# Kernel optimization log

Hardware: AMD Instinct MI355X
Metric: run time of the kernel (lower is better)

## Reference

```python
import jax, jax.numpy as jnp
import numpy as np

EPS = 1e-5

def _segment_mean(src_feat, edge_index, num_targets):
    # src_feat: [Ns, D]; edge_index: [2, E] = [source_idx, target_idx]
    msgs = src_feat[edge_index[0]]                                   # [E, D] gather
    agg = jax.ops.segment_sum(msgs, edge_index[1], num_segments=num_targets)
    deg = jax.ops.segment_sum(jnp.ones((edge_index.shape[1],), src_feat.dtype),
                              edge_index[1], num_segments=num_targets)
    return agg / jnp.clip(deg, 1.0)[:, None]

def _layernorm(x, gamma, beta):
    mu = jnp.mean(x, axis=-1, keepdims=True)
    var = jnp.mean(jnp.square(x - mu), axis=-1, keepdims=True)
    return (x - mu) * jax.lax.rsqrt(var + EPS) * gamma + beta

def setup_inputs() -> dict:
    key = jax.random.key(0)
    ks = jax.random.split(key, 8)
    NU, NI, E, D = 50000, 50000, 300000, 256
    s = 1.0 / np.sqrt(D)
    return {
        "user_features": jax.random.normal(ks[0], (NU, D), jnp.float32),
        "item_features": jax.random.normal(ks[1], (NI, D), jnp.float32),
        "user_item_edge_index": jax.random.randint(ks[2], (2, E), 0, NI),
        "item_user_edge_index": jax.random.randint(ks[3], (2, E), 0, NU),
        "Wu": jax.random.uniform(ks[4], (D, D), jnp.float32, -s, s),
        "bu": jax.random.uniform(ks[5], (D,), jnp.float32, -s, s),
        "Wi": jax.random.uniform(ks[6], (D, D), jnp.float32, -s, s),
        "bi": jax.random.uniform(ks[7], (D,), jnp.float32, -s, s),
        "gamma": jnp.ones((D,), jnp.float32),
        "beta": jnp.zeros((D,), jnp.float32),
    }

def reference(user_features, item_features, user_item_edge_index, item_user_edge_index,
              Wu, bu, Wi, bi, gamma, beta):
    num_items = item_features.shape[0]
    num_users = user_features.shape[0]
    # messages into items come from users; into users come from items
    item_messages = _segment_mean(user_features, user_item_edge_index, num_items)
    user_messages = _segment_mean(item_features, item_user_edge_index, num_users)
    u_new = (user_features + user_messages) @ Wu + bu
    i_new = (item_features + item_messages) @ Wi + bi
    u_new = _layernorm(jax.nn.relu(u_new), gamma, beta)
    i_new = _layernorm(jax.nn.relu(i_new), gamma, beta)
    return (u_new, i_new)
```

## Files before the change

### kernel.cpp

```cpp
#include <hip/hip_runtime.h>
#include <hip/hip_bf16.h>

#define D 256
#define BM 64
#define BK2 32
#define LDK2 40
#define LDK 72

typedef __attribute__((ext_vector_type(8))) __bf16 bf16x8;
typedef __attribute__((ext_vector_type(4))) float f32x4;

__device__ __forceinline__ float bf2f(unsigned short u) {
    union { unsigned int i; float f; } c; c.i = ((unsigned int)u) << 16; return c.f;
}
__device__ __forceinline__ float bf2f_lo(unsigned int u) {
    union { unsigned int i; float f; } c; c.i = u << 16; return c.f;
}
__device__ __forceinline__ float bf2f_hi(unsigned int u) {
    union { unsigned int i; float f; } c; c.i = u & 0xffff0000u; return c.f;
}
__device__ __forceinline__ unsigned short f2bf(float f) {
    __hip_bfloat16 h = __float2bfloat16(f);
    return *reinterpret_cast<unsigned short*>(&h);
}
__device__ __forceinline__ unsigned int pack2(float lo, float hi) {
    return (unsigned int)f2bf(lo) | ((unsigned int)f2bf(hi) << 16);
}


__global__ void k_cvt_all(const float* __restrict__ uf, const float* __restrict__ itf,
                          const float* __restrict__ Wu, const float* __restrict__ Wi,
                          unsigned short* __restrict__ feat_bf,
                          unsigned short* __restrict__ Wt_u, unsigned short* __restrict__ Wt_i,
                          int* __restrict__ deg, int Ntot,
                          size_t nfU, size_t nfTot, int nbF) {
    int b = blockIdx.x;
    if (b < nbF) {
        size_t base = ((size_t)b * 256 + threadIdx.x) * 8;
        if (base < nfTot) {
            const float* s = (base < nfU) ? (uf + base) : (itf + (base - nfU));
            float4 f0 = *(const float4*)s;
            float4 f1 = *(const float4*)(s + 4);
            ushort4 o0, o1;
            o0.x = f2bf(f0.x); o0.y = f2bf(f0.y); o0.z = f2bf(f0.z); o0.w = f2bf(f0.w);
            o1.x = f2bf(f1.x); o1.y = f2bf(f1.y); o1.z = f2bf(f1.z); o1.w = f2bf(f1.w);
            ((ushort4*)(feat_bf + base))[0] = o0;
            ((ushort4*)(feat_bf + base))[1] = o1;
        }
    } else if (b < nbF + 512) {
        int b2 = b - nbF;
        const float* W = (b2 < 256) ? Wu : Wi;
        unsigned short* Wt = (b2 < 256) ? Wt_u : Wt_i;
        int k = b2 & 255;
        int c = threadIdx.x;
        Wt[(size_t)c * 256 + k] = f2bf(W[(size_t)k * 256 + c]);
    } else {
        int zb = b - nbF - 512;
        size_t base = ((size_t)zb * 256 + threadIdx.x) * 4;
        if (base + 4 <= (size_t)Ntot) {
            *(int4*)(deg + base) = make_int4(0, 0, 0, 0);
        } else if (base < (size_t)Ntot) {
            for (size_t j = base; j < (size_t)Ntot; ++j) deg[j] = 0;
        }
    }
}

__global__ void k_hist2(const int* __restrict__ iu_e, int Eiu,
                        const int* __restrict__ ui_e, int Eui,
                        int* __restrict__ deg, int NU) {
    int e = blockIdx.x * blockDim.x + threadIdx.x;
    if (e < Eiu) {
        atomicAdd(&deg[iu_e[Eiu + e]], 1);
    } else if (e < Eiu + Eui) {
        int e2 = e - Eiu;
        atomicAdd(&deg[NU + ui_e[Eui + e2]], 1);
    }
}

__global__ void k_scan_block(const int* __restrict__ deg, int N,
                             int* __restrict__ rs, int* __restrict__ bsums) {
    __shared__ int s[1024];
    int base = blockIdx.x * 1024;
    int t = threadIdx.x;
    int v = (base + t < N) ? deg[base + t] : 0;
    s[t] = v;
    __syncthreads();
    for (int off = 1; off < 1024; off <<= 1) {
        int add = (t >= off) ? s[t - off] : 0;
        __syncthreads();
        s[t] += add;
        __syncthreads();
    }
    if (base + t < N) rs[base + t + 1] = s[t];
    if (t == 1023) bsums[blockIdx.x] = s[1023];
}

__global__ void k_scan_sums(int* __restrict__ bsums, int nb) {
    __shared__ int s[1024];
    int t = threadIdx.x;
    int v = (t < nb) ? bsums[t] : 0;
    s[t] = v;
    __syncthreads();
    for (int off = 1; off < 1024; off <<= 1) {
        int add = (t >= off) ? s[t - off] : 0;
        __syncthreads();
        s[t] += add;
        __syncthreads();
    }
    if (t < nb) bsums[t] = s[t] - v;
}

__global__ void k_finalize(int N, int* __restrict__ rs, int* __restrict__ cur,
                           const int* __restrict__ bsums) {
    int i = blockIdx.x * blockDim.x + threadIdx.x;
    if (i < N) {
        int v = rs[i + 1] + bsums[i >> 10];
        rs[i + 1] = v;
        cur[i + 1] = v;
    }
    if (i == 0) { rs[0] = 0; cur[0] = 0; }
}

__global__ void k_fill2(const int* __restrict__ iu_e, int Eiu,
                        const int* __restrict__ ui_e, int Eui,
                        int* __restrict__ cur, int NU,
                        int* __restrict__ csr) {
    int e = blockIdx.x * blockDim.x + threadIdx.x;
    if (e < Eiu) {
        int d = iu_e[Eiu + e];
        int p = atomicAdd(&cur[d], 1);
        csr[p] = iu_e[e];
    } else if (e < Eiu + Eui) {
        int e2 = e - Eiu;
        int d = ui_e[Eui + e2];
        int p = atomicAdd(&cur[NU + d], 1);
        csr[p] = ui_e[e2];
    }
}

__global__ void k_msg2(const unsigned short* __restrict__ uf_bf,
                       const unsigned short* __restrict__ if_bf,
                       const int* __restrict__ rs, const int* __restrict__ csr,
                       unsigned short* __restrict__ x_u, unsigned short* __restrict__ x_i,
                       int NU, int NI) {
    int pair = (blockIdx.x * blockDim.x + threadIdx.x) >> 6;
    int lane = threadIdx.x & 63;
    int half = lane >> 5;
    int hl   = lane & 31;
    int Ntot = NU + NI;
    int wv = pair * 2 + half;
    if (wv >= Ntot) return;

    const unsigned short* src; const unsigned short* tgt; unsigned short* xo; int w;
    if (wv < NU) { src = if_bf; tgt = uf_bf; xo = x_u; w = wv; }
    else         { src = uf_bf; tgt = if_bf; xo = x_i; w = wv - NU; }

    int s0 = rs[wv], s1 = rs[wv + 1];
    float a0[8] = {}, a1[8] = {}, a2[8] = {}, a3[8] = {};

    int i = s0;
    for (; i + 4 <= s1; i += 4) {
        int e0 = csr[i], e1 = csr[i + 1], e2 = csr[i + 2], e3 = csr[i + 3];
        uint4 r0 = ((const uint4*)(src + (size_t)e0 * D))[hl];
        uint4 r1 = ((const uint4*)(src + (size_t)e1 * D))[hl];
        uint4 r2 = ((const uint4*)(src + (size_t)e2 * D))[hl];
        uint4 r3 = ((const uint4*)(src + (size_t)e3 * D))[hl];
        a0[0] += bf2f_lo(r0.x); a0[1] += bf2f_hi(r0.x); a0[2] += bf2f_lo(r0.y); a0[3] += bf2f_hi(r0.y);
        a0[4] += bf2f_lo(r0.z); a0[5] += bf2f_hi(r0.z); a0[6] += bf2f_lo(r0.w); a0[7] += bf2f_hi(r0.w);
        a1[0] += bf2f_lo(r1.x); a1[1] += bf2f_hi(r1.x); a1[2] += bf2f_lo(r1.y); a1[3] += bf2f_hi(r1.y);
        a1[4] += bf2f_lo(r1.z); a1[5] += bf2f_hi(r1.z); a1[6] += bf2f_lo(r1.w); a1[7] += bf2f_hi(r1.w);
        a2[0] += bf2f_lo(r2.x); a2[1] += bf2f_hi(r2.x); a2[2] += bf2f_lo(r2.y); a2[3] += bf2f_hi(r2.y);
        a2[4] += bf2f_lo(r2.z); a2[5] += bf2f_hi(r2.z); a2[6] += bf2f_lo(r2.w); a2[7] += bf2f_hi(r2.w);
        a3[0] += bf2f_lo(r3.x); a3[1] += bf2f_hi(r3.x); a3[2] += bf2f_lo(r3.y); a3[3] += bf2f_hi(r3.y);
        a3[4] += bf2f_lo(r3.z); a3[5] += bf2f_hi(r3.z); a3[6] += bf2f_lo(r3.w); a3[7] += bf2f_hi(r3.w);
    }
    for (; i < s1; ++i) {
        int e0 = csr[i];
        uint4 r0 = ((const uint4*)(src + (size_t)e0 * D))[hl];
        a0[0] += bf2f_lo(r0.x); a0[1] += bf2f_hi(r0.x); a0[2] += bf2f_lo(r0.y); a0[3] += bf2f_hi(r0.y);
        a0[4] += bf2f_lo(r0.z); a0[5] += bf2f_hi(r0.z); a0[6] += bf2f_lo(r0.w); a0[7] += bf2f_hi(r0.w);
    }

    int cnt = s1 - s0;
    float inv = 1.0f / (float)(cnt > 0 ? cnt : 1);
    uint4 tv = ((const uint4*)(tgt + (size_t)w * D))[hl];
    float x0 = bf2f_lo(tv.x) + (a0[0] + a1[0] + a2[0] + a3[0]) * inv;
    float x1 = bf2f_hi(tv.x) + (a0[1] + a1[1] + a2[1] + a3[1]) * inv;
    float x2 = bf2f_lo(tv.y) + (a0[2] + a1[2] + a2[2] + a3[2]) * inv;
    float x3 = bf2f_hi(tv.y) + (a0[3] + a1[3] + a2[3] + a3[3]) * inv;
    float x4 = bf2f_lo(tv.z) + (a0[4] + a1[4] + a2[4] + a3[4]) * inv;
    float x5 = bf2f_hi(tv.z) + (a0[5] + a1[5] + a2[5] + a3[5]) * inv;
    float x6 = bf2f_lo(tv.w) + (a0[6] + a1[6] + a2[6] + a3[6]) * inv;
    float x7 = bf2f_hi(tv.w) + (a0[7] + a1[7] + a2[7] + a3[7]) * inv;
    uint4 o;
    o.x = pack2(x0, x1); o.y = pack2(x2, x3); o.z = pack2(x4, x5); o.w = pack2(x6, x7);
    ((uint4*)(xo + (size_t)w * D))[hl] = o;
}

__launch_bounds__(256)
__global__ void k_gemm2(const unsigned short* __restrict__ x_u,
                        const unsigned short* __restrict__ x_i,
                        const unsigned short* __restrict__ Wt_u,
                        const unsigned short* __restrict__ Wt_i,
                        const float* __restrict__ bu, const float* __restrict__ bi,
                        const float* __restrict__ gamma, const float* __restrict__ beta,
                        int NU, int NI, int nbU, float* __restrict__ out) {
    __shared__ __hip_bfloat16 As[BM][LDK2];
    __shared__ __hip_bfloat16 Bs[D][LDK2];
    __shared__ float red_s[BM][4];
    __shared__ float red_q[BM][4];

    int b = blockIdx.x;
    bool isU = b < nbU;
    const unsigned short* X  = isU ? x_u : x_i;
    const unsigned short* Wt = isU ? Wt_u : Wt_i;
    const float* bias        = isU ? bu : bi;
    float* Y                 = isU ? out : out + (size_t)NU * D;
    int N                    = isU ? NU : NI;
    int row0 = (isU ? b : b - nbU) * BM;

    int t = threadIdx.x;
    int lane = t & 63;
    int w = t >> 6;
    int l15 = lane & 15;
    int l4 = lane >> 4;

    int ar = row0 + (t >> 2);
    int ak = (t & 3) * 8;
    const uint4* Ag = (const uint4*)&X[(size_t)ar * D + ak];
    const uint4* Bg = (const uint4*)&Wt[(size_t)t * D];

    uint4 uz = {0, 0, 0, 0};
    bool aok = (ar < N);
    uint4 aR = aok ? Ag[0] : uz;
    uint4 bR0 = Bg[0], bR1 = Bg[1], bR2 = Bg[2], bR3 = Bg[3];

    f32x4 acc[4][4];
    f32x4 zero = {0.f, 0.f, 0.f, 0.f};
    #pragma unroll
    for (int fr = 0; fr < 4; fr++)
        #pragma unroll
        for (int fc = 0; fc < 4; fc++)
            acc[fr][fc] = zero;

    for (int k0 = 0; k0 < D; k0 += BK2) {
        *(uint4*)&As[t >> 2][ak] = aR;
        *(uint4*)&Bs[t][0]  = bR0;
        *(uint4*)&Bs[t][8]  = bR1;
        *(uint4*)&Bs[t][16] = bR2;
        *(uint4*)&Bs[t][24] = bR3;
        __syncthreads();
        if (k0 + BK2 < D) {
            int kn = (k0 + BK2) >> 3;
            aR  = aok ? Ag[kn] : uz;
            bR0 = Bg[kn]; bR1 = Bg[kn + 1]; bR2 = Bg[kn + 2]; bR3 = Bg[kn + 3];
        }
        bf16x8 af[4], bg4[4];
        #pragma unroll
        for (int fr = 0; fr < 4; fr++)
            af[fr] = *(const bf16x8*)&As[fr * 16 + l15][l4 * 8];
        #pragma unroll
        for (int fc = 0; fc < 4; fc++)
            bg4[fc] = *(const bf16x8*)&Bs[w * 64 + fc * 16 + l15][l4 * 8];
        #pragma unroll
        for (int fr = 0; fr < 4; fr++)
            #pragma unroll
            for (int fc = 0; fc < 4; fc++)
                acc[fr][fc] = __builtin_amdgcn_mfma_f32_16x16x32_bf16(
                    af[fr], bg4[fc], acc[fr][fc], 0, 0, 0);
        __syncthreads();
    }

    float bias_c[4], gam_c[4], bet_c[4];
    #pragma unroll
    for (int fc = 0; fc < 4; fc++) {
        int col = w * 64 + fc * 16 + l15;
        bias_c[fc] = bias[col];
        gam_c[fc]  = gamma[col];
        bet_c[fc]  = beta[col];
    }

    #pragma unroll
    for (int fr = 0; fr < 4; fr++) {
        #pragma unroll
        for (int r = 0; r < 4; r++) {
            int row = fr * 16 + l4 * 4 + r;
            float s = 0.f, q = 0.f;
            #pragma unroll
            for (int fc = 0; fc < 4; fc++) {
                float v = acc[fr][fc][r] + bias_c[fc];
                v = fmaxf(v, 0.f);
                acc[fr][fc][r] = v;
                s += v;
                q += v * v;
            }
            #pragma unroll
            for (int m = 1; m < 16; m <<= 1) {
                s += __shfl_xor(s, m);
                q += __shfl_xor(q, m);
            }
            if (l15 == 0) { red_s[row][w] = s; red_q[row][w] = q; }
        }
    }
    __syncthreads();

    #pragma unroll
    for (int fr = 0; fr < 4; fr++) {
        #pragma unroll
        for (int r = 0; r < 4; r++) {
            int row = fr * 16 + l4 * 4 + r;
            int grow = row0 + row;
            if (grow >= N) continue;
            float s = red_s[row][0] + red_s[row][1] + red_s[row][2] + red_s[row][3];
            float q = red_q[row][0] + red_q[row][1] + red_q[row][2] + red_q[row][3];
            float mu  = s * (1.0f / 256.0f);
            float var = q * (1.0f / 256.0f) - mu * mu;
            float rstd = rsqrtf(var + 1e-5f);
            #pragma unroll
            for (int fc = 0; fc < 4; fc++) {
                int col = w * 64 + fc * 16 + l15;
                Y[(size_t)grow * D + col] = (acc[fr][fc][r] - mu) * rstd * gam_c[fc] + bet_c[fc];
            }
        }
    }
}


__global__ void k_hist(const int* __restrict__ dst, int E, int* __restrict__ deg) {
    int e = blockIdx.x * blockDim.x + threadIdx.x;
    if (e < E) atomicAdd(&deg[dst[e]], 1);
}

__global__ void k_finalize_rs(int N, int* __restrict__ rs, const int* __restrict__ bsums) {
    int i = blockIdx.x * blockDim.x + threadIdx.x;
    if (i < N) rs[i + 1] += bsums[i >> 10];
    if (i == 0) rs[0] = 0;
}

__global__ void k_fill(const int* __restrict__ src, const int* __restrict__ dst, int E,
                       const int* __restrict__ rs, int* __restrict__ cursor,
                       int* __restrict__ csr) {
    int e = blockIdx.x * blockDim.x + threadIdx.x;
    if (e < E) {
        int d = dst[e];
        int p = atomicAdd(&cursor[d], 1);
        csr[rs[d] + p] = src[e];
    }
}

__global__ void k_msg_x(const float* __restrict__ srcf, const float* __restrict__ tgtf,
                        const int* __restrict__ rs, const int* __restrict__ csr,
                        int N, float* __restrict__ xout) {
    int wave = (blockIdx.x * blockDim.x + threadIdx.x) >> 6;
    int lane = threadIdx.x & 63;
    if (wave >= N) return;
    int s0 = rs[wave], s1 = rs[wave + 1];
    float4 acc = make_float4(0.f, 0.f, 0.f, 0.f);
    for (int i = s0; i < s1; i++) {
        int s = csr[i];
        float4 f = *(const float4*)&srcf[(size_t)s * D + lane * 4];
        acc.x += f.x; acc.y += f.y; acc.z += f.z; acc.w += f.w;
    }
    int cnt = s1 - s0;
    float inv = 1.0f / (float)(cnt > 0 ? cnt : 1);
    float4 t = *(const float4*)&tgtf[(size_t)wave * D + lane * 4];
    float4 x;
    x.x = t.x + acc.x * inv;
    x.y = t.y + acc.y * inv;
    x.z = t.z + acc.z * inv;
    x.w = t.w + acc.w * inv;
    *(float4*)&xout[(size_t)wave * D + lane * 4] = x;
}

__global__ void k_wcvt(const float* __restrict__ W0, const float* __restrict__ W1,
                       __hip_bfloat16* __restrict__ Wt0, __hip_bfloat16* __restrict__ Wt1) {
    int b = blockIdx.x;
    const float* W = (b < 256) ? W0 : W1;
    __hip_bfloat16* Wt = (b < 256) ? Wt0 : Wt1;
    int k = b & 255;
    int c = threadIdx.x;
    Wt[(size_t)c * 256 + k] = __float2bfloat16(W[(size_t)k * 256 + c]);
}

__launch_bounds__(256)
__global__ void k_gemm_mfma_ln(const float* __restrict__ X,
                               const __hip_bfloat16* __restrict__ Wt,
                               const float* __restrict__ bias,
                               const float* __restrict__ gamma,
                               const float* __restrict__ beta,
                               int N, float* __restrict__ Y) {
    __shared__ __hip_bfloat16 As[BM][LDK];
    __shared__ __hip_bfloat16 Bs[D][LDK];
    __shared__ float red_s[BM][4];
    __shared__ float red_q[BM][4];

    int t = threadIdx.x;
    int lane = t & 63;
    int w = t >> 6;
    int l15 = lane & 15;
    int l4 = lane >> 4;
    int row0 = blockIdx.x * BM;

    f32x4 acc[4][4];
    f32x4 zero = {0.f, 0.f, 0.f, 0.f};
    #pragma unroll
    for (int fr = 0; fr < 4; fr++)
        #pragma unroll
        for (int fc = 0; fc < 4; fc++)
            acc[fr][fc] = zero;

    for (int k0 = 0; k0 < D; k0 += 64) {
        {
            int i = t >> 2;
            int kq = (t & 3) * 16;
            int r = row0 + i;
            float4 f[4];
            if (r < N) {
                const float4* p = (const float4*)&X[(size_t)r * D + k0 + kq];
                f[0] = p[0]; f[1] = p[1]; f[2] = p[2]; f[3] = p[3];
            } else {
                float4 z4 = make_float4(0.f, 0.f, 0.f, 0.f);
                f[0] = z4; f[1] = z4; f[2] = z4; f[3] = z4;
            }
            __hip_bfloat16 vb[16];
            #pragma unroll
            for (int q = 0; q < 4; q++) {
                vb[q * 4 + 0] = __float2bfloat16(f[q].x);
                vb[q * 4 + 1] = __float2bfloat16(f[q].y);
                vb[q * 4 + 2] = __float2bfloat16(f[q].z);
                vb[q * 4 + 3] = __float2bfloat16(f[q].w);
            }
            *(uint4*)&As[i][kq]     = *(uint4*)&vb[0];
            *(uint4*)&As[i][kq + 8] = *(uint4*)&vb[8];
        }
        #pragma unroll
        for (int pass = 0; pass < 4; pass++) {
            int c = pass * 64 + (t >> 2);
            int kq = (t & 3) * 16;
            const uint4* p = (const uint4*)&Wt[(size_t)c * D + k0 + kq];
            uint4 b0 = p[0], b1 = p[1];
            *(uint4*)&Bs[c][kq]     = b0;
            *(uint4*)&Bs[c][kq + 8] = b1;
        }
        __syncthreads();

        #pragma unroll
        for (int ks = 0; ks < 2; ks++) {
            bf16x8 af[4], bg[4];
            #pragma unroll
            for (int fr = 0; fr < 4; fr++)
                af[fr] = *(const bf16x8*)&As[fr * 16 + l15][ks * 32 + l4 * 8];
            #pragma unroll
            for (int fc = 0; fc < 4; fc++)
                bg[fc] = *(const bf16x8*)&Bs[w * 64 + fc * 16 + l15][ks * 32 + l4 * 8];
            #pragma unroll
            for (int fr = 0; fr < 4; fr++)
                #pragma unroll
                for (int fc = 0; fc < 4; fc++)
                    acc[fr][fc] = __builtin_amdgcn_mfma_f32_16x16x32_bf16(
                        af[fr], bg[fc], acc[fr][fc], 0, 0, 0);
        }
        __syncthreads();
    }

    float bias_c[4], gam_c[4], bet_c[4];
    #pragma unroll
    for (int fc = 0; fc < 4; fc++) {
        int col = w * 64 + fc * 16 + l15;
        bias_c[fc] = bias[col];
        gam_c[fc]  = gamma[col];
        bet_c[fc]  = beta[col];
    }

    #pragma unroll
    for (int fr = 0; fr < 4; fr++) {
        #pragma unroll
        for (int r = 0; r < 4; r++) {
            int row = fr * 16 + l4 * 4 + r;
            float s = 0.f, q = 0.f;
            #pragma unroll
            for (int fc = 0; fc < 4; fc++) {
                float v = acc[fr][fc][r] + bias_c[fc];
                v = fmaxf(v, 0.f);
                acc[fr][fc][r] = v;
                s += v;
                q += v * v;
            }
            #pragma unroll
            for (int m = 1; m < 16; m <<= 1) {
                s += __shfl_xor(s, m);
                q += __shfl_xor(q, m);
            }
            if (l15 == 0) { red_s[row][w] = s; red_q[row][w] = q; }
        }
    }
    __syncthreads();

    #pragma unroll
    for (int fr = 0; fr < 4; fr++) {
        #pragma unroll
        for (int r = 0; r < 4; r++) {
            int row = fr * 16 + l4 * 4 + r;
            int grow = row0 + row;
            if (grow >= N) continue;
            float s = red_s[row][0] + red_s[row][1] + red_s[row][2] + red_s[row][3];
            float q = red_q[row][0] + red_q[row][1] + red_q[row][2] + red_q[row][3];
            float mu  = s * (1.0f / 256.0f);
            float var = q * (1.0f / 256.0f) - mu * mu;
            float rstd = rsqrtf(var + 1e-5f);
            #pragma unroll
            for (int fc = 0; fc < 4; fc++) {
                int col = w * 64 + fc * 16 + l15;
                Y[(size_t)grow * D + col] = (acc[fr][fc][r] - mu) * rstd * gam_c[fc] + bet_c[fc];
            }
        }
    }
}


extern "C" void kernel_launch(void* const* d_in, const int* in_sizes, int n_in,
                              void* d_out, int out_size, void* d_ws, size_t ws_size,
                              hipStream_t stream) {
    const float* uf    = (const float*)d_in[0];
    const float* itf   = (const float*)d_in[1];
    const int*   ui_e  = (const int*)d_in[2];
    const int*   iu_e  = (const int*)d_in[3];
    const float* Wu    = (const float*)d_in[4];
    const float* bu    = (const float*)d_in[5];
    const float* Wi    = (const float*)d_in[6];
    const float* bi    = (const float*)d_in[7];
    const float* gamma = (const float*)d_in[8];
    const float* beta  = (const float*)d_in[9];

    int NU  = in_sizes[0] / D;
    int NI  = in_sizes[1] / D;
    int Eui = in_sizes[2] / 2;
    int Eiu = in_sizes[3] / 2;
    int Nmax = NU > NI ? NU : NI;
    int Ntot = NU + NI;
    int Etot = Eiu + Eui;

    float* out   = (float*)d_out;
    size_t nfU = (size_t)NU * D;
    size_t nfI = (size_t)NI * D;
    size_t nfTot = nfU + nfI;

    unsigned short* uf_bf = (unsigned short*)d_ws;
    unsigned short* if_bf = uf_bf + nfU;
    unsigned short* x_u   = if_bf + nfI;
    unsigned short* x_i   = x_u + nfU;
    unsigned short* Wt_u2 = x_i + nfI;
    unsigned short* Wt_i2 = Wt_u2 + 65536;
    int* deg2  = (int*)(Wt_i2 + 65536);
    int* rs2   = deg2 + Ntot;
    int* cur2  = rs2 + Ntot + 1;
    int* bsums = cur2 + Ntot + 1;
    int* csr2  = bsums + 1024;
    size_t needed = (size_t)((char*)(csr2 + Etot) - (char*)d_ws);

    if (ws_size >= needed) {
        int nbF = (int)((nfTot + 2047) / 2048);
        int nbZ = (Ntot + 1023) / 1024;
        k_cvt_all<<<nbF + 512 + nbZ, 256, 0, stream>>>(uf, itf, Wu, Wi, uf_bf, Wt_u2, Wt_i2,
                                                       deg2, Ntot, nfU, nfTot, nbF);
        k_hist2<<<(Etot + 255) / 256, 256, 0, stream>>>(iu_e, Eiu, ui_e, Eui, deg2, NU);
        int nb = (Ntot + 1023) / 1024;
        k_scan_block<<<nb, 1024, 0, stream>>>(deg2, Ntot, rs2, bsums);
        k_scan_sums<<<1, 1024, 0, stream>>>(bsums, nb);
        k_finalize<<<(Ntot + 255) / 256, 256, 0, stream>>>(Ntot, rs2, cur2, bsums);
        k_fill2<<<(Etot + 255) / 256, 256, 0, stream>>>(iu_e, Eiu, ui_e, Eui, cur2, NU, csr2);
        int pairs = (Ntot + 1) / 2;
        k_msg2<<<(pairs + 3) / 4, 256, 0, stream>>>(uf_bf, if_bf, rs2, csr2, x_u, x_i, NU, NI);
        int nbU = (NU + BM - 1) / BM;
        int nbI = (NI + BM - 1) / BM;
        k_gemm2<<<nbU + nbI, 256, 0, stream>>>(x_u, x_i, Wt_u2, Wt_i2, bu, bi, gamma, beta,
                                               NU, NI, nbU, out);
        return;
    }

    float* u_out = out;
    float* i_out = out + nfU;
    __hip_bfloat16* Wt_u = (__hip_bfloat16*)d_ws;
    __hip_bfloat16* Wt_i = Wt_u + 256 * 256;
    int* deg    = (int*)(Wt_i + 256 * 256);
    int* rs     = deg + Nmax;
    int* bs     = rs + Nmax + 1;
    int* cursor = bs + 1024;
    int* csr    = cursor + Nmax;

    k_wcvt<<<512, 256, 0, stream>>>(Wu, Wi, Wt_u, Wt_i);

    auto run_side = [&](const float* srcf, const float* tgtf, const int* edges, int E,
                        int N, const __hip_bfloat16* Wt, const float* bias, float* y) {
        const int* esrc = edges;
        const int* edst = edges + E;
        hipMemsetAsync(deg, 0, (size_t)N * sizeof(int), stream);
        hipMemsetAsync(cursor, 0, (size_t)N * sizeof(int), stream);
        k_hist<<<(E + 255) / 256, 256, 0, stream>>>(edst, E, deg);
        int nb = (N + 1023) / 1024;
        k_scan_block<<<nb, 1024, 0, stream>>>(deg, N, rs, bs);
        k_scan_sums<<<1, 1024, 0, stream>>>(bs, nb);
        k_finalize_rs<<<(N + 255) / 256, 256, 0, stream>>>(N, rs, bs);
        k_fill<<<(E + 255) / 256, 256, 0, stream>>>(esrc, edst, E, rs, cursor, csr);
        k_msg_x<<<(N + 3) / 4, 256, 0, stream>>>(srcf, tgtf, rs, csr, N, y);
        k_gemm_mfma_ln<<<(N + BM - 1) / BM, 256, 0, stream>>>(y, Wt, bias, gamma, beta, N, y);
    };

    run_side(itf, uf, iu_e, Eiu, NU, Wt_u, bu, u_out);
    run_side(uf, itf, ui_e, Eui, NI, Wt_i, bi, i_out);
}
```

Baseline: 219.2 us.

## Fuse neighbor aggregation into GEMM+LayerNorm kernel and merge histogram into prep

The gather-mean aggregation now runs inside the GEMM kernel, writing each 64-row tile of combined features straight into shared memory instead of materialising x_u/x_i in global memory. B operands are read directly from global memory per k-step, with no shared-memory staging. The output is staged through LDS so each row is written as coalesced float4 stores. The degree histogram moves into the prep kernel, with a memset for zeroing. This removes a full bf16 intermediate round-trip and some launches, but the GEMM blocks now do irregular gathers that may hurt occupancy (about 33KB LDS per block).

New measurement: 240.9 us. +9.9%, slower.

```diff
diff --git a/kernel.cpp b/kernel.cpp
--- a/kernel.cpp
+++ b/kernel.cpp
@@ -3,8 +3,8 @@
 
 #define D 256
 #define BM 64
-#define BK2 32
-#define LDK2 40
+#define LDA 264
+#define LDAF 260
 #define LDK 72
 
 typedef __attribute__((ext_vector_type(8))) __bf16 bf16x8;
@@ -28,12 +28,14 @@
 }
 
 
-__global__ void k_cvt_all(const float* __restrict__ uf, const float* __restrict__ itf,
-                          const float* __restrict__ Wu, const float* __restrict__ Wi,
-                          unsigned short* __restrict__ feat_bf,
-                          unsigned short* __restrict__ Wt_u, unsigned short* __restrict__ Wt_i,
-                          int* __restrict__ deg, int Ntot,
-                          size_t nfU, size_t nfTot, int nbF) {
+__global__ void k_prep(const float* __restrict__ uf, const float* __restrict__ itf,
+                       const float* __restrict__ Wu, const float* __restrict__ Wi,
+                       unsigned short* __restrict__ feat_bf,
+                       unsigned short* __restrict__ Wt_u, unsigned short* __restrict__ Wt_i,
+                       const int* __restrict__ iu_e, int Eiu,
+                       const int* __restrict__ ui_e, int Eui,
+                       int* __restrict__ deg, int NU,
+                       size_t nfU, size_t nfTot, int nbF) {
     int b = blockIdx.x;
     if (b < nbF) {
         size_t base = ((size_t)b * 256 + threadIdx.x) * 8;
@@ -55,25 +57,13 @@
         int c = threadIdx.x;
         Wt[(size_t)c * 256 + k] = f2bf(W[(size_t)k * 256 + c]);
     } else {
-        int zb = b - nbF - 512;
-        size_t base = ((size_t)zb * 256 + threadIdx.x) * 4;
-        if (base + 4 <= (size_t)Ntot) {
-            *(int4*)(deg + base) = make_int4(0, 0, 0, 0);
-        } else if (base < (size_t)Ntot) {
-            for (size_t j = base; j < (size_t)Ntot; ++j) deg[j] = 0;
-        }
-    }
-}
-
-__global__ void k_hist2(const int* __restrict__ iu_e, int Eiu,
-                        const int* __restrict__ ui_e, int Eui,
-                        int* __restrict__ deg, int NU) {
-    int e = blockIdx.x * blockDim.x + threadIdx.x;
-    if (e < Eiu) {
-        atomicAdd(&deg[iu_e[Eiu + e]], 1);
-    } else if (e < Eiu + Eui) {
-        int e2 = e - Eiu;
-        atomicAdd(&deg[NU + ui_e[Eui + e2]], 1);
+        int e = (b - nbF - 512) * 256 + threadIdx.x;
+        if (e < Eiu) {
+            atomicAdd(&deg[iu_e[Eiu + e]], 1);
+        } else if (e < Eiu + Eui) {
+            int e2 = e - Eiu;
+            atomicAdd(&deg[NU + ui_e[Eui + e2]], 1);
+        }
     }
 }
 
@@ -138,102 +128,86 @@
     }
 }
 
-__global__ void k_msg2(const unsigned short* __restrict__ uf_bf,
-                       const unsigned short* __restrict__ if_bf,
-                       const int* __restrict__ rs, const int* __restrict__ csr,
-                       unsigned short* __restrict__ x_u, unsigned short* __restrict__ x_i,
-                       int NU, int NI) {
-    int pair = (blockIdx.x * blockDim.x + threadIdx.x) >> 6;
-    int lane = threadIdx.x & 63;
-    int half = lane >> 5;
-    int hl   = lane & 31;
-    int Ntot = NU + NI;
-    int wv = pair * 2 + half;
-    if (wv >= Ntot) return;
-
-    const unsigned short* src; const unsigned short* tgt; unsigned short* xo; int w;
-    if (wv < NU) { src = if_bf; tgt = uf_bf; xo = x_u; w = wv; }
-    else         { src = uf_bf; tgt = if_bf; xo = x_i; w = wv - NU; }
-
-    int s0 = rs[wv], s1 = rs[wv + 1];
-    float a0[8] = {}, a1[8] = {}, a2[8] = {}, a3[8] = {};
-
-    int i = s0;
-    for (; i + 4 <= s1; i += 4) {
-        int e0 = csr[i], e1 = csr[i + 1], e2 = csr[i + 2], e3 = csr[i + 3];
-        uint4 r0 = ((const uint4*)(src + (size_t)e0 * D))[hl];
-        uint4 r1 = ((const uint4*)(src + (size_t)e1 * D))[hl];
-        uint4 r2 = ((const uint4*)(src + (size_t)e2 * D))[hl];
-        uint4 r3 = ((const uint4*)(src + (size_t)e3 * D))[hl];
-        a0[0] += bf2f_lo(r0.x); a0[1] += bf2f_hi(r0.x); a0[2] += bf2f_lo(r0.y); a0[3] += bf2f_hi(r0.y);
-        a0[4] += bf2f_lo(r0.z); a0[5] += bf2f_hi(r0.z); a0[6] += bf2f_lo(r0.w); a0[7] += bf2f_hi(r0.w);
-        a1[0] += bf2f_lo(r1.x); a1[1] += bf2f_hi(r1.x); a1[2] += bf2f_lo(r1.y); a1[3] += bf2f_hi(r1.y);
-        a1[4] += bf2f_lo(r1.z); a1[5] += bf2f_hi(r1.z); a1[6] += bf2f_lo(r1.w); a1[7] += bf2f_hi(r1.w);
-        a2[0] += bf2f_lo(r2.x); a2[1] += bf2f_hi(r2.x); a2[2] += bf2f_lo(r2.y); a2[3] += bf2f_hi(r2.y);
-        a2[4] += bf2f_lo(r2.z); a2[5] += bf2f_hi(r2.z); a2[6] += bf2f_lo(r2.w); a2[7] += bf2f_hi(r2.w);
-        a3[0] += bf2f_lo(r3.x); a3[1] += bf2f_hi(r3.x); a3[2] += bf2f_lo(r3.y); a3[3] += bf2f_hi(r3.y);
-        a3[4] += bf2f_lo(r3.z); a3[5] += bf2f_hi(r3.z); a3[6] += bf2f_lo(r3.w); a3[7] += bf2f_hi(r3.w);
-    }
-    for (; i < s1; ++i) {
-        int e0 = csr[i];
-        uint4 r0 = ((const uint4*)(src + (size_t)e0 * D))[hl];
-        a0[0] += bf2f_lo(r0.x); a0[1] += bf2f_hi(r0.x); a0[2] += bf2f_lo(r0.y); a0[3] += bf2f_hi(r0.y);
-        a0[4] += bf2f_lo(r0.z); a0[5] += bf2f_hi(r0.z); a0[6] += bf2f_lo(r0.w); a0[7] += bf2f_hi(r0.w);
-    }
-
-    int cnt = s1 - s0;
-    float inv = 1.0f / (float)(cnt > 0 ? cnt : 1);
-    uint4 tv = ((const uint4*)(tgt + (size_t)w * D))[hl];
-    float x0 = bf2f_lo(tv.x) + (a0[0] + a1[0] + a2[0] + a3[0]) * inv;
-    float x1 = bf2f_hi(tv.x) + (a0[1] + a1[1] + a2[1] + a3[1]) * inv;
-    float x2 = bf2f_lo(tv.y) + (a0[2] + a1[2] + a2[2] + a3[2]) * inv;
-    float x3 = bf2f_hi(tv.y) + (a0[3] + a1[3] + a2[3] + a3[3]) * inv;
-    float x4 = bf2f_lo(tv.z) + (a0[4] + a1[4] + a2[4] + a3[4]) * inv;
-    float x5 = bf2f_hi(tv.z) + (a0[5] + a1[5] + a2[5] + a3[5]) * inv;
-    float x6 = bf2f_lo(tv.w) + (a0[6] + a1[6] + a2[6] + a3[6]) * inv;
-    float x7 = bf2f_hi(tv.w) + (a0[7] + a1[7] + a2[7] + a3[7]) * inv;
-    uint4 o;
-    o.x = pack2(x0, x1); o.y = pack2(x2, x3); o.z = pack2(x4, x5); o.w = pack2(x6, x7);
-    ((uint4*)(xo + (size_t)w * D))[hl] = o;
-}
-
 __launch_bounds__(256)
-__global__ void k_gemm2(const unsigned short* __restrict__ x_u,
-                        const unsigned short* __restrict__ x_i,
+__global__ void k_fused(const unsigned short* __restrict__ uf_bf,
+                        const unsigned short* __restrict__ if_bf,
                         const unsigned short* __restrict__ Wt_u,
                         const unsigned short* __restrict__ Wt_i,
+                        const int* __restrict__ rs, const int* __restrict__ csr,
                         const float* __restrict__ bu, const float* __restrict__ bi,
                         const float* __restrict__ gamma, const float* __restrict__ beta,
                         int NU, int NI, int nbU, float* __restrict__ out) {
-    __shared__ __hip_bfloat16 As[BM][LDK2];
-    __shared__ __hip_bfloat16 Bs[D][LDK2];
+    __shared__ __align__(16) __hip_bfloat16 As[BM][LDA];
     __shared__ float red_s[BM][4];
     __shared__ float red_q[BM][4];
 
     int b = blockIdx.x;
     bool isU = b < nbU;
-    const unsigned short* X  = isU ? x_u : x_i;
-    const unsigned short* Wt = isU ? Wt_u : Wt_i;
-    const float* bias        = isU ? bu : bi;
-    float* Y                 = isU ? out : out + (size_t)NU * D;
-    int N                    = isU ? NU : NI;
+    const unsigned short* srcT = isU ? if_bf : uf_bf;
+    const unsigned short* tgtT = isU ? uf_bf : if_bf;
+    const unsigned short* Wt   = isU ? Wt_u : Wt_i;
+    const float* bias          = isU ? bu : bi;
+    float* Y                   = isU ? out : out + (size_t)NU * D;
+    int N                      = isU ? NU : NI;
     int row0 = (isU ? b : b - nbU) * BM;
+    int wvBase = (isU ? 0 : NU) + row0;
 
     int t = threadIdx.x;
     int lane = t & 63;
     int w = t >> 6;
     int l15 = lane & 15;
     int l4 = lane >> 4;
-
-    int ar = row0 + (t >> 2);
-    int ak = (t & 3) * 8;
-    const uint4* Ag = (const uint4*)&X[(size_t)ar * D + ak];
-    const uint4* Bg = (const uint4*)&Wt[(size_t)t * D];
-
-    uint4 uz = {0, 0, 0, 0};
-    bool aok = (ar < N);
-    uint4 aR = aok ? Ag[0] : uz;
-    uint4 bR0 = Bg[0], bR1 = Bg[1], bR2 = Bg[2], bR3 = Bg[3];
+    int half = lane >> 5;
+    int hl = lane & 31;
+
+    for (int it = 0; it < 8; ++it) {
+        int lrow = (it * 4 + w) * 2 + half;
+        int grow = row0 + lrow;
+        if (grow < N) {
+            int wv = wvBase + lrow;
+            int s0 = rs[wv], s1 = rs[wv + 1];
+            float a0[8] = {}, a1[8] = {}, a2[8] = {}, a3[8] = {};
+            int i = s0;
+            for (; i + 4 <= s1; i += 4) {
+                int e0 = csr[i], e1 = csr[i + 1], e2 = csr[i + 2], e3 = csr[i + 3];
+                uint4 r0 = ((const uint4*)(srcT + (size_t)e0 * D))[hl];
+                uint4 r1 = ((const uint4*)(srcT + (size_t)e1 * D))[hl];
+                uint4 r2 = ((const uint4*)(srcT + (size_t)e2 * D))[hl];
+                uint4 r3 = ((const uint4*)(srcT + (size_t)e3 * D))[hl];
+                a0[0] += bf2f_lo(r0.x); a0[1] += bf2f_hi(r0.x); a0[2] += bf2f_lo(r0.y); a0[3] += bf2f_hi(r0.y);
+                a0[4] += bf2f_lo(r0.z); a0[5] += bf2f_hi(r0.z); a0[6] += bf2f_lo(r0.w); a0[7] += bf2f_hi(r0.w);
+                a1[0] += bf2f_lo(r1.x); a1[1] += bf2f_hi(r1.x); a1[2] += bf2f_lo(r1.y); a1[3] += bf2f_hi(r1.y);
+                a1[4] += bf2f_lo(r1.z); a1[5] += bf2f_hi(r1.z); a1[6] += bf2f_lo(r1.w); a1[7] += bf2f_hi(r1.w);
+                a2[0] += bf2f_lo(r2.x); a2[1] += bf2f_hi(r2.x); a2[2] += bf2f_lo(r2.y); a2[3] += bf2f_hi(r2.y);
+                a2[4] += bf2f_lo(r2.z); a2[5] += bf2f_hi(r2.z); a2[6] += bf2f_lo(r2.w); a2[7] += bf2f_hi(r2.w);
+                a3[0] += bf2f_lo(r3.x); a3[1] += bf2f_hi(r3.x); a3[2] += bf2f_lo(r3.y); a3[3] += bf2f_hi(r3.y);
+                a3[4] += bf2f_lo(r3.z); a3[5] += bf2f_hi(r3.z); a3[6] += bf2f_lo(r3.w); a3[7] += bf2f_hi(r3.w);
+            }
+            for (; i < s1; ++i) {
+                int e0 = csr[i];
+                uint4 r0 = ((const uint4*)(srcT + (size_t)e0 * D))[hl];
+                a0[0] += bf2f_lo(r0.x); a0[1] += bf2f_hi(r0.x); a0[2] += bf2f_lo(r0.y); a0[3] += bf2f_hi(r0.y);
+                a0[4] += bf2f_lo(r0.z); a0[5] += bf2f_hi(r0.z); a0[6] += bf2f_lo(r0.w); a0[7] += bf2f_hi(r0.w);
+            }
+            int cnt = s1 - s0;
+            float inv = 1.0f / (float)(cnt > 0 ? cnt : 1);
+            uint4 tv = ((const uint4*)(tgtT + (size_t)grow * D))[hl];
+            float x0 = bf2f_lo(tv.x) + (a0[0] + a1[0] + a2[0] + a3[0]) * inv;
+            float x1 = bf2f_hi(tv.x) + (a0[1] + a1[1] + a2[1] + a3[1]) * inv;
+            float x2 = bf2f_lo(tv.y) + (a0[2] + a1[2] + a2[2] + a3[2]) * inv;
+            float x3 = bf2f_hi(tv.y) + (a0[3] + a1[3] + a2[3] + a3[3]) * inv;
+            float x4 = bf2f_lo(tv.z) + (a0[4] + a1[4] + a2[4] + a3[4]) * inv;
+            float x5 = bf2f_hi(tv.z) + (a0[5] + a1[5] + a2[5] + a3[5]) * inv;
+            float x6 = bf2f_lo(tv.w) + (a0[6] + a1[6] + a2[6] + a3[6]) * inv;
+            float x7 = bf2f_hi(tv.w) + (a0[7] + a1[7] + a2[7] + a3[7]) * inv;
+            uint4 o;
+            o.x = pack2(x0, x1); o.y = pack2(x2, x3); o.z = pack2(x4, x5); o.w = pack2(x6, x7);
+            *(uint4*)&As[lrow][hl * 8] = o;
+        } else {
+            uint4 z = {0, 0, 0, 0};
+            *(uint4*)&As[lrow][hl * 8] = z;
+        }
+    }
 
     f32x4 acc[4][4];
     f32x4 zero = {0.f, 0.f, 0.f, 0.f};
@@ -243,32 +217,26 @@
         for (int fc = 0; fc < 4; fc++)
             acc[fr][fc] = zero;
 
-    for (int k0 = 0; k0 < D; k0 += BK2) {
-        *(uint4*)&As[t >> 2][ak] = aR;
-        *(uint4*)&Bs[t][0]  = bR0;
-        *(uint4*)&Bs[t][8]  = bR1;
-        *(uint4*)&Bs[t][16] = bR2;
-        *(uint4*)&Bs[t][24] = bR3;
-        __syncthreads();
-        if (k0 + BK2 < D) {
-            int kn = (k0 + BK2) >> 3;
-            aR  = aok ? Ag[kn] : uz;
-            bR0 = Bg[kn]; bR1 = Bg[kn + 1]; bR2 = Bg[kn + 2]; bR3 = Bg[kn + 3];
-        }
-        bf16x8 af[4], bg4[4];
-        #pragma unroll
-        for (int fr = 0; fr < 4; fr++)
-            af[fr] = *(const bf16x8*)&As[fr * 16 + l15][l4 * 8];
-        #pragma unroll
-        for (int fc = 0; fc < 4; fc++)
-            bg4[fc] = *(const bf16x8*)&Bs[w * 64 + fc * 16 + l15][l4 * 8];
-        #pragma unroll
-        for (int fr = 0; fr < 4; fr++)
-            #pragma unroll
-            for (int fc = 0; fc < 4; fc++)
+    __syncthreads();
+
+    const uint4* Bg = (const uint4*)Wt;
+    int colB = w * 64 + l15;
+    #pragma unroll
+    for (int ks8 = 0; ks8 < 8; ++ks8) {
+        uint4 bq[4];
+        #pragma unroll
+        for (int fc = 0; fc < 4; ++fc)
+            bq[fc] = Bg[(size_t)(colB + fc * 16) * 32 + ks8 * 4 + l4];
+        bf16x8 af[4];
+        #pragma unroll
+        for (int fr = 0; fr < 4; ++fr)
+            af[fr] = *(const bf16x8*)&As[fr * 16 + l15][ks8 * 32 + l4 * 8];
+        #pragma unroll
+        for (int fr = 0; fr < 4; ++fr)
+            #pragma unroll
+            for (int fc = 0; fc < 4; ++fc)
                 acc[fr][fc] = __builtin_amdgcn_mfma_f32_16x16x32_bf16(
-                    af[fr], bg4[fc], acc[fr][fc], 0, 0, 0);
-        __syncthreads();
+                    af[fr], *(bf16x8*)&bq[fc], acc[fr][fc], 0, 0, 0);
     }
 
     float bias_c[4], gam_c[4], bet_c[4];
@@ -304,24 +272,38 @@
     }
     __syncthreads();
 
-    #pragma unroll
-    for (int fr = 0; fr < 4; fr++) {
-        #pragma unroll
-        for (int r = 0; r < 4; r++) {
-            int row = fr * 16 + l4 * 4 + r;
-            int grow = row0 + row;
-            if (grow >= N) continue;
-            float s = red_s[row][0] + red_s[row][1] + red_s[row][2] + red_s[row][3];
-            float q = red_q[row][0] + red_q[row][1] + red_q[row][2] + red_q[row][3];
-            float mu  = s * (1.0f / 256.0f);
-            float var = q * (1.0f / 256.0f) - mu * mu;
-            float rstd = rsqrtf(var + 1e-5f);
-            #pragma unroll
-            for (int fc = 0; fc < 4; fc++) {
-                int col = w * 64 + fc * 16 + l15;
-                Y[(size_t)grow * D + col] = (acc[fr][fc][r] - mu) * rstd * gam_c[fc] + bet_c[fc];
-            }
-        }
+    float* AsF = (float*)&As[0][0];
+    for (int h = 0; h < 2; ++h) {
+        #pragma unroll
+        for (int fr2 = 0; fr2 < 2; ++fr2) {
+            int fr = h * 2 + fr2;
+            #pragma unroll
+            for (int r = 0; r < 4; ++r) {
+                int row = fr * 16 + l4 * 4 + r;
+                float s = red_s[row][0] + red_s[row][1] + red_s[row][2] + red_s[row][3];
+                float q = red_q[row][0] + red_q[row][1] + red_q[row][2] + red_q[row][3];
+                float mu  = s * (1.0f / 256.0f);
+                float var = q * (1.0f / 256.0f) - mu * mu;
+                float rstd = rsqrtf(var + 1e-5f);
+                int lr = row - h * 32;
+                #pragma unroll
+                for (int fc = 0; fc < 4; ++fc) {
+                    int col = w * 64 + fc * 16 + l15;
+                    AsF[lr * LDAF + col] = (acc[fr][fc][r] - mu) * rstd * gam_c[fc] + bet_c[fc];
+                }
+            }
+        }
+        __syncthreads();
+        #pragma unroll
+        for (int j = 0; j < 8; ++j) {
+            int r = j * 4 + w;
+            int grow = row0 + h * 32 + r;
+            if (grow < N) {
+                float4 v = *(float4*)&AsF[r * LDAF + lane * 4];
+                *(float4*)&Y[(size_t)grow * D + lane * 4] = v;
+            }
+        }
+        __syncthreads();
     }
 }
 
@@ -547,9 +529,7 @@
 
     unsigned short* uf_bf = (unsigned short*)d_ws;
     unsigned short* if_bf = uf_bf + nfU;
-    unsigned short* x_u   = if_bf + nfI;
-    unsigned short* x_i   = x_u + nfU;
-    unsigned short* Wt_u2 = x_i + nfI;
+    unsigned short* Wt_u2 = if_bf + nfI;
     unsigned short* Wt_i2 = Wt_u2 + 65536;
     int* deg2  = (int*)(Wt_i2 + 65536);
     int* rs2   = deg2 + Ntot;
@@ -560,21 +540,20 @@
 
     if (ws_size >= needed) {
         int nbF = (int)((nfTot + 2047) / 2048);
-        int nbZ = (Ntot + 1023) / 1024;
-        k_cvt_all<<<nbF + 512 + nbZ, 256, 0, stream>>>(uf, itf, Wu, Wi, uf_bf, Wt_u2, Wt_i2,
-                                                       deg2, Ntot, nfU, nfTot, nbF);
-        k_hist2<<<(Etot + 255) / 256, 256, 0, stream>>>(iu_e, Eiu, ui_e, Eui, deg2, NU);
+        int nbH = (Etot + 255) / 256;
+        hipMemsetAsync(deg2, 0, (size_t)Ntot * sizeof(int), stream);
+        k_prep<<<nbF + 512 + nbH, 256, 0, stream>>>(uf, itf, Wu, Wi, uf_bf, Wt_u2, Wt_i2,
+                                                    iu_e, Eiu, ui_e, Eui, deg2, NU,
+                                                    nfU, nfTot, nbF);
         int nb = (Ntot + 1023) / 1024;
         k_scan_block<<<nb, 1024, 0, stream>>>(deg2, Ntot, rs2, bsums);
         k_scan_sums<<<1, 1024, 0, stream>>>(bsums, nb);
         k_finalize<<<(Ntot + 255) / 256, 256, 0, stream>>>(Ntot, rs2, cur2, bsums);
-        k_fill2<<<(Etot + 255) / 256, 256, 0, stream>>>(iu_e, Eiu, ui_e, Eui, cur2, NU, csr2);
-        int pairs = (Ntot + 1) / 2;
-        k_msg2<<<(pairs + 3) / 4, 256, 0, stream>>>(uf_bf, if_bf, rs2, csr2, x_u, x_i, NU, NI);
+        k_fill2<<<nbH, 256, 0, stream>>>(iu_e, Eiu, ui_e, Eui, cur2, NU, csr2);
         int nbU = (NU + BM - 1) / BM;
         int nbI = (NI + BM - 1) / BM;
-        k_gemm2<<<nbU + nbI, 256, 0, stream>>>(x_u, x_i, Wt_u2, Wt_i2, bu, bi, gamma, beta,
-                                               NU, NI, nbU, out);
+        k_fused<<<nbU + nbI, 256, 0, stream>>>(uf_bf, if_bf, Wt_u2, Wt_i2, rs2, csr2,
+                                               bu, bi, gamma, beta, NU, NI, nbU, out);
         return;
     }
 
```
